# Kernel tuning notes

Hardware: AMD Instinct MI355X
Metric: run time of the kernel (lower is better)

Reference implementation:

```python
import jax, jax.numpy as jnp
import numpy as np

N_NODES = 50000
N_EDGES = 800000


def setup_inputs() -> dict:
    key = jax.random.key(0)
    k1, k2, k3, k4 = jax.random.split(key, 4)
    x = jax.random.normal(k1, (N_NODES, 100), dtype=jnp.float32)
    edge_index = jax.random.randint(k2, (2, N_EDGES), 0, N_NODES, dtype=jnp.int64)
    W1 = jax.random.normal(k3, (100, 128), dtype=jnp.float32) * 0.1
    b1 = jnp.zeros((128,), dtype=jnp.float32)
    W2 = jax.random.normal(k4, (128, 64), dtype=jnp.float32) * 0.1
    b2 = jnp.zeros((64,), dtype=jnp.float32)
    return {"x": x, "edge_index": edge_index, "W1": W1, "b1": b1, "W2": W2, "b2": b2}


def _gcn_norm(edge_index, n_nodes):
    # PyG GCNConv default: add self-loops, then symmetric normalization
    row, col = edge_index[0], edge_index[1]
    loop = jnp.arange(n_nodes, dtype=row.dtype)
    row = jnp.concatenate([row, loop])
    col = jnp.concatenate([col, loop])
    deg = jax.ops.segment_sum(jnp.ones_like(col, dtype=jnp.float32), col,
                              num_segments=n_nodes)
    dinv = jnp.where(deg > 0, jax.lax.rsqrt(deg), 0.0)
    norm = dinv[row] * dinv[col]  # [E + N]
    return row, col, norm


def _gcn_conv(x, W, b, row, col, norm, n_nodes):
    h = x @ W                       # [N, out] linear transform first (PyG order)
    msg = norm[:, None] * h[row]    # gather + scale over edges
    agg = jax.ops.segment_sum(msg, col, num_segments=n_nodes)  # scatter-add
    return agg + b


def reference(x, edge_index, W1, b1, W2, b2):
    n = x.shape[0]
    row, col, norm = _gcn_norm(edge_index, n)
    h = _gcn_conv(x, W1, b1, row, col, norm, n)
    h = jax.nn.relu(h)
    out = _gcn_conv(h, W2, b2, row, col, norm, n)
    return out
```

## Files before the change

kernel.cpp:

```cpp
#include <hip/hip_runtime.h>
#include <hip/hip_fp16.h>

#define DIV_UP(a,b) (((a)+(b)-1)/(b))

typedef _Float16 half8 __attribute__((ext_vector_type(8)));
typedef float f32x4 __attribute__((ext_vector_type(4)));

#define BUK_BITS 9
#define BUK_SIZE 512
#define BUK_CAP  12288
#define MAXBUK   128
#define NBLK_BUCKET 512
#define CHUNK_MAX 1568

#define SWZ(row, colh) ((colh) ^ (((row) & 7) << 3))


__device__ __forceinline__ int edge_at(const void* ei, int mode64, int idx) {
  if (mode64) return (int)((const long long*)ei)[idx];
  return ((const int*)ei)[idx];
}

__global__ void k_init(const int* __restrict__ ei32, int* __restrict__ mode,
                       int* __restrict__ bcur, int nbuk) {
  int t = threadIdx.x;
  if (t < 64) {
    int v = ei32[2 * t + 1];
    unsigned long long b = __ballot(v == 0);
    if (t == 0) *mode = (b == ~0ull) ? 1 : 0;
  }
  if (t < nbuk) bcur[t] = t * BUK_CAP;
}

__global__ __launch_bounds__(256) void k_bucket(const void* __restrict__ ei,
                                                const int* __restrict__ mode,
                                                int* __restrict__ bcur,
                                                unsigned int* __restrict__ recs,
                                                int E, int nbuk) {
  __shared__ unsigned int lrec[CHUNK_MAX];
  __shared__ unsigned int sorted[CHUNK_MAX];
  __shared__ int hist[MAXBUK], lofs[MAXBUK], gbase[MAXBUK], cur[MAXBUK];

  const int chunk = DIV_UP(E, gridDim.x);
  const int e0 = blockIdx.x * chunk;
  const int cnt = min(E, e0 + chunk) - e0;
  if (cnt <= 0) return;

  for (int i = threadIdx.x; i < nbuk; i += 256) hist[i] = 0;
  __syncthreads();

  const int m = *mode;
  for (int i = threadIdx.x; i < cnt; i += 256) {
    int r = edge_at(ei, m, e0 + i);
    int c = edge_at(ei, m, E + e0 + i);
    unsigned int rec = ((unsigned)c << 16) | (unsigned)r;
    lrec[i] = rec;
    atomicAdd(&hist[c >> BUK_BITS], 1);
  }
  __syncthreads();

  if (threadIdx.x == 0) {
    int run = 0;
    for (int b = 0; b < nbuk; ++b) { lofs[b] = run; run += hist[b]; }
  }
  __syncthreads();
  for (int b = threadIdx.x; b < nbuk; b += 256) {
    gbase[b] = atomicAdd(&bcur[b], hist[b]);
    cur[b] = lofs[b];
  }
  __syncthreads();

  for (int i = threadIdx.x; i < cnt; i += 256) {
    unsigned int rec = lrec[i];
    int b = rec >> (16 + BUK_BITS);
    int p = atomicAdd(&cur[b], 1);
    sorted[p] = rec;
  }
  __syncthreads();

  for (int i = threadIdx.x; i < cnt; i += 256) {
    unsigned int rec = sorted[i];
    int b = rec >> (16 + BUK_BITS);
    recs[gbase[b] + i - lofs[b]] = rec;
  }
}

__global__ __launch_bounds__(256) void k_bdeg(const int* __restrict__ bcur,
                                              const unsigned int* __restrict__ recs,
                                              float* __restrict__ dinv,
                                              int* __restrict__ rowstart,
                                              int n, int E, int nbuk) {
  __shared__ int h[BUK_SIZE];
  __shared__ int psum[256];
  __shared__ int cnts[MAXBUK];
  __shared__ int sbase;
  const int b = blockIdx.x, tid = threadIdx.x;

  if (tid < nbuk) cnts[tid] = bcur[tid] - tid * BUK_CAP;
  h[tid] = 0; h[tid + 256] = 0;
  __syncthreads();
  if (tid == 0) { int s = 0; for (int j = 0; j < b; ++j) s += cnts[j]; sbase = s; }
  const int cnt = cnts[b];
  const int n0 = b << BUK_BITS;
  const int nn = min(BUK_SIZE, n - n0);
  const int base = b * BUK_CAP;

  for (int i = tid; i < cnt; i += 256)
    atomicAdd(&h[(int)(recs[base + i] >> 16) - n0], 1);
  __syncthreads();

  int a0 = h[2 * tid], a1 = h[2 * tid + 1];
  psum[tid] = a0 + a1;
  __syncthreads();
#pragma unroll
  for (int off2 = 1; off2 < 256; off2 <<= 1) {
    int v = (tid >= off2) ? psum[tid - off2] : 0;
    __syncthreads();
    psum[tid] += v;
    __syncthreads();
  }
  int excl = psum[tid] - (a0 + a1);
  int gb = sbase;
  if (2 * tid < nn)     rowstart[n0 + 2 * tid]     = gb + excl;
  if (2 * tid + 1 < nn) rowstart[n0 + 2 * tid + 1] = gb + excl + a0;
  for (int i = tid; i < nn; i += 256)
    dinv[n0 + i] = rsqrtf((float)h[i] + 1.0f);
  if (b == nbuk - 1 && tid == 0) rowstart[n] = E;
}

__global__ __launch_bounds__(256) void k_convx(const float4* __restrict__ x4,
                                               const float* __restrict__ dinv,
                                               uint2* __restrict__ xh4, int total4) {
  int i = blockIdx.x * 256 + threadIdx.x;
  if (i < total4) {
    int node = i / 25;
    float d = dinv[node];
    float4 v = x4[i];
    union { uint2 u; __half2 h[2]; } p;
    p.h[0] = __halves2half2(__float2half_rn(d * v.x), __float2half_rn(d * v.y));
    p.h[1] = __halves2half2(__float2half_rn(d * v.z), __float2half_rn(d * v.w));
    xh4[i] = p.u;
  }
}

__global__ __launch_bounds__(256) void k_convw2(const float* __restrict__ W1,
                                                const float* __restrict__ W2,
                                                _Float16* __restrict__ Wt1,
                                                _Float16* __restrict__ Wt2) {
  int i = blockIdx.x * 256 + threadIdx.x;
  if (i < 128 * 128) {
    int nn = i >> 7, k = i & 127;
    Wt1[i] = (k < 100) ? (_Float16)W1[k * 128 + nn] : (_Float16)0.f;
  } else if (i < 128 * 128 + 64 * 128) {
    int j = i - 128 * 128;
    int nn = j >> 7, k = j & 127;
    Wt2[j] = (_Float16)W2[k * 64 + nn];
  }
}

__global__ __launch_bounds__(256) void k_csrfill(const int* __restrict__ bcur,
                                                 const unsigned int* __restrict__ recs,
                                                 const int* __restrict__ rowstart,
                                                 unsigned short* __restrict__ csr, int n) {
  __shared__ unsigned short lcsr[BUK_CAP];
  __shared__ int curs[BUK_SIZE];
  const int b = blockIdx.x;
  const int base = b * BUK_CAP;
  const int cnt = bcur[b] - base;
  const int n0 = b << BUK_BITS;
  const int nn = min(BUK_SIZE, n - n0);
  const int sec0 = rowstart[n0];

  for (int i = threadIdx.x; i < nn; i += 256) curs[i] = rowstart[n0 + i] - sec0;
  __syncthreads();
  for (int i = threadIdx.x; i < cnt; i += 256) {
    unsigned int rec = recs[base + i];
    int cl = (int)(rec >> 16) - n0;
    int p = atomicAdd(&curs[cl], 1);
    lcsr[p] = (unsigned short)(rec & 0xFFFFu);
  }
  __syncthreads();
  for (int i = threadIdx.x; i < cnt; i += 256) csr[sec0 + i] = lcsr[i];
}

__device__ __forceinline__ float4 h4_to_f4(uint2 u) {
  union { uint2 u; __half2 h[2]; } p; p.u = u;
  float2 a = __half22float2(p.h[0]);
  float2 b = __half22float2(p.h[1]);
  return make_float4(a.x, a.y, b.x, b.y);
}
__device__ __forceinline__ void acc_add(float4& acc, float4 a) {
  acc.x += a.x; acc.y += a.y; acc.z += a.z; acc.w += a.w;
}

__global__ __launch_bounds__(256) void k_pull1(const int* __restrict__ rowstart,
                                               const unsigned short* __restrict__ csr,
                                               const uint2* __restrict__ xh4,
                                               const float* __restrict__ dinv,
                                               uint2* __restrict__ aggh4, int n) {
  int g = threadIdx.x / 25;
  int lane = threadIdx.x - g * 25;
  if (g >= 10) return;
  int node = blockIdx.x * 10 + g;
  if (node >= n) return;

  float4 acc = h4_to_f4(xh4[node * 25 + lane]);
  int beg = rowstart[node], end = rowstart[node + 1];
  int j = beg;
  for (; j + 3 < end; j += 4) {
    int r0 = csr[j], r1 = csr[j + 1], r2 = csr[j + 2], r3 = csr[j + 3];
    float4 a = h4_to_f4(xh4[r0 * 25 + lane]);
    float4 b = h4_to_f4(xh4[r1 * 25 + lane]);
    float4 c = h4_to_f4(xh4[r2 * 25 + lane]);
    float4 d = h4_to_f4(xh4[r3 * 25 + lane]);
    acc_add(acc, a); acc_add(acc, b); acc_add(acc, c); acc_add(acc, d);
  }
  for (; j < end; ++j) acc_add(acc, h4_to_f4(xh4[(int)csr[j] * 25 + lane]));

  float d = dinv[node];
  union { uint2 u; __half2 h[2]; } p;
  p.h[0] = __halves2half2(__float2half_rn(d * acc.x), __float2half_rn(d * acc.y));
  p.h[1] = __halves2half2(__float2half_rn(d * acc.z), __float2half_rn(d * acc.w));
  aggh4[node * 32 + lane] = p.u;
  if (lane < 7) aggh4[node * 32 + 25 + lane] = make_uint2(0u, 0u);
}

__global__ __launch_bounds__(256) void k_pull2(const int* __restrict__ rowstart,
                                               const unsigned short* __restrict__ csr,
                                               const uint4* __restrict__ th4,
                                               const float* __restrict__ dinv,
                                               const float4* __restrict__ b2_4,
                                               float4* __restrict__ out4, int n) {
  int g = threadIdx.x >> 3;
  int lane = threadIdx.x & 7;
  int node = blockIdx.x * 32 + g;
  if (node >= n) return;

  uint4 sv = th4[node * 8 + lane];
  float4 acc0 = h4_to_f4(make_uint2(sv.x, sv.y));
  float4 acc1 = h4_to_f4(make_uint2(sv.z, sv.w));

  int beg = rowstart[node], end = rowstart[node + 1];
  int j = beg;
  for (; j + 3 < end; j += 4) {
    uint4 u0 = th4[(int)csr[j] * 8 + lane];
    uint4 u1 = th4[(int)csr[j + 1] * 8 + lane];
    uint4 u2 = th4[(int)csr[j + 2] * 8 + lane];
    uint4 u3 = th4[(int)csr[j + 3] * 8 + lane];
    acc_add(acc0, h4_to_f4(make_uint2(u0.x, u0.y)));
    acc_add(acc1, h4_to_f4(make_uint2(u0.z, u0.w)));
    acc_add(acc0, h4_to_f4(make_uint2(u1.x, u1.y)));
    acc_add(acc1, h4_to_f4(make_uint2(u1.z, u1.w)));
    acc_add(acc0, h4_to_f4(make_uint2(u2.x, u2.y)));
    acc_add(acc1, h4_to_f4(make_uint2(u2.z, u2.w)));
    acc_add(acc0, h4_to_f4(make_uint2(u3.x, u3.y)));
    acc_add(acc1, h4_to_f4(make_uint2(u3.z, u3.w)));
  }
  for (; j < end; ++j) {
    uint4 u0 = th4[(int)csr[j] * 8 + lane];
    acc_add(acc0, h4_to_f4(make_uint2(u0.x, u0.y)));
    acc_add(acc1, h4_to_f4(make_uint2(u0.z, u0.w)));
  }
  float d = dinv[node];
  float4 bb0 = b2_4[lane * 2], bb1 = b2_4[lane * 2 + 1];
  out4[node * 16 + lane * 2]     = make_float4(d * acc0.x + bb0.x, d * acc0.y + bb0.y,
                                               d * acc0.z + bb0.z, d * acc0.w + bb0.w);
  out4[node * 16 + lane * 2 + 1] = make_float4(d * acc1.x + bb1.x, d * acc1.y + bb1.y,
                                               d * acc1.z + bb1.z, d * acc1.w + bb1.w);
}

__global__ __launch_bounds__(256, 2) void k_gemmf(const _Float16* __restrict__ A,
                                                  const _Float16* __restrict__ Wt1,
                                                  const float* __restrict__ b1,
                                                  const _Float16* __restrict__ Wt2,
                                                  const float* __restrict__ dinv,
                                                  _Float16* __restrict__ thh, int n) {
  __shared__ __align__(16) _Float16 lds[4][16 * 128];
  const int wid = threadIdx.x >> 6;
  const int lane = threadIdx.x & 63;
  const int lr = lane & 15;
  const int lk = lane >> 4;
  _Float16* myl = lds[wid];

  half8 B1[8][4];
#pragma unroll
  for (int nt = 0; nt < 8; ++nt)
#pragma unroll
    for (int ks = 0; ks < 4; ++ks)
      B1[nt][ks] = *(const half8*)&Wt1[(nt * 16 + lr) * 128 + ks * 32 + lk * 8];
  float bs[8];
#pragma unroll
  for (int nt = 0; nt < 8; ++nt) bs[nt] = b1[nt * 16 + lr];

  const int nstrips = (n + 15) >> 4;
  for (int s = blockIdx.x * 4 + wid; s < nstrips; s += gridDim.x * 4) {
    const int arow = s * 16 + lr;
    half8 a[4];
#pragma unroll
    for (int ks = 0; ks < 4; ++ks)
      a[ks] = (arow < n) ? *(const half8*)&A[(size_t)arow * 128 + ks * 32 + lk * 8]
                         : half8{0, 0, 0, 0, 0, 0, 0, 0};
    f32x4 acc[8];
#pragma unroll
    for (int nt = 0; nt < 8; ++nt) acc[nt] = f32x4{0.f, 0.f, 0.f, 0.f};
#pragma unroll
    for (int ks = 0; ks < 4; ++ks)
#pragma unroll
      for (int nt = 0; nt < 8; ++nt)
        acc[nt] = __builtin_amdgcn_mfma_f32_16x16x32_f16(a[ks], B1[nt][ks], acc[nt], 0, 0, 0);

#pragma unroll
    for (int r = 0; r < 4; ++r) {
      int row = lk * 4 + r;
#pragma unroll
      for (int nt = 0; nt < 8; ++nt)
        myl[row * 128 + SWZ(row, nt * 16 + lr)] =
            (_Float16)fmaxf(acc[nt][r] + bs[nt], 0.f);
    }

    half8 B2[4][4];
#pragma unroll
    for (int nt = 0; nt < 4; ++nt)
#pragma unroll
      for (int ks = 0; ks < 4; ++ks)
        B2[nt][ks] = *(const half8*)&Wt2[(nt * 16 + lr) * 128 + ks * 32 + lk * 8];

    half8 a2[4];
#pragma unroll
    for (int ks = 0; ks < 4; ++ks)
      a2[ks] = *(const half8*)&myl[lr * 128 + SWZ(lr, ks * 32 + lk * 8)];

    f32x4 acc2[4];
#pragma unroll
    for (int nt = 0; nt < 4; ++nt) acc2[nt] = f32x4{0.f, 0.f, 0.f, 0.f};
#pragma unroll
    for (int ks = 0; ks < 4; ++ks)
#pragma unroll
      for (int nt = 0; nt < 4; ++nt)
        acc2[nt] = __builtin_amdgcn_mfma_f32_16x16x32_f16(a2[ks], B2[nt][ks], acc2[nt], 0, 0, 0);

    const int rb = s * 16 + lk * 4;
    float sc[4];
    if (rb + 3 < n) {
      const float4 dv = *(const float4*)&dinv[rb];
      sc[0] = dv.x; sc[1] = dv.y; sc[2] = dv.z; sc[3] = dv.w;
    } else {
#pragma unroll
      for (int r = 0; r < 4; ++r) sc[r] = (rb + r < n) ? dinv[rb + r] : 0.f;
    }
#pragma unroll
    for (int r = 0; r < 4; ++r) {
      const int orow = rb + r;
      if (orow < n) {
#pragma unroll
        for (int nt = 0; nt < 4; ++nt)
          thh[(size_t)orow * 64 + nt * 16 + lr] = (_Float16)(acc2[nt][r] * sc[r]);
      }
    }
  }
}

extern "C" void kernel_launch(void* const* d_in, const int* in_sizes, int n_in,
                              void* d_out, int out_size, void* d_ws, size_t ws_size,
                              hipStream_t stream) {
  const float* x  = (const float*)d_in[0];
  const void*  ei = d_in[1];
  const float* W1 = (const float*)d_in[2];
  const float* b1 = (const float*)d_in[3];
  const float* W2 = (const float*)d_in[4];
  const float* b2 = (const float*)d_in[5];
  float* out = (float*)d_out;

  const int n = in_sizes[0] / 100;
  const int E = in_sizes[1] / 2;
  const int nbuk = DIV_UP(n, BUK_SIZE);

  char* ws = (char*)d_ws;
  size_t off = 0;
  auto alloc = [&](size_t bytes) { void* p = ws + off; off += (bytes + 15) & ~15ull; return p; };
  int*            mode     = (int*)   alloc(64 * 4);
  int*            bcur     = (int*)   alloc(MAXBUK * 4);
  float*          dinv     = (float*) alloc((size_t)n * 4);
  int*            rowstart = (int*)   alloc(((size_t)n + 4) * 4);
  unsigned int*   recs     = (unsigned int*)alloc((size_t)nbuk * BUK_CAP * 4);
  unsigned short* csr      = (unsigned short*)alloc((size_t)E * 2);
  _Float16*       xh       = (_Float16*)alloc((size_t)n * 100 * 2);
  _Float16*       aggh     = (_Float16*)alloc((size_t)n * 128 * 2);
  _Float16*       thh      = (_Float16*)alloc((size_t)n * 64 * 2);
  _Float16*       Wt1h     = (_Float16*)alloc(128 * 128 * 2);
  _Float16*       Wt2h     = (_Float16*)alloc(64 * 128 * 2);

  k_init<<<1, 128, 0, stream>>>((const int*)ei, mode, bcur, nbuk);
  k_bucket<<<NBLK_BUCKET, 256, 0, stream>>>(ei, mode, bcur, recs, E, nbuk);
  k_bdeg<<<nbuk, 256, 0, stream>>>(bcur, recs, dinv, rowstart, n, E, nbuk);

  k_convx<<<DIV_UP(n * 25, 256), 256, 0, stream>>>((const float4*)x, dinv, (uint2*)xh, n * 25);
  k_convw2<<<DIV_UP(128 * 128 + 64 * 128, 256), 256, 0, stream>>>(W1, W2, Wt1h, Wt2h);
  k_csrfill<<<nbuk, 256, 0, stream>>>(bcur, recs, rowstart, csr, n);

  k_pull1<<<DIV_UP(n, 10), 256, 0, stream>>>(rowstart, csr, (const uint2*)xh, dinv,
                                             (uint2*)aggh, n);
  const int nstrips = DIV_UP(n, 16);
  k_gemmf<<<DIV_UP(nstrips, 8), 256, 0, stream>>>(aggh, Wt1h, b1, Wt2h, dinv, thh, n);
  k_pull2<<<DIV_UP(n, 32), 256, 0, stream>>>(rowstart, csr, (const uint4*)thh, dinv,
                                             (const float4*)b2, (float4*)out, n);
}
```

Baseline: 132.0 us.

## Pad CSR rows to multiples of eight with dummy node, fuse degree and fill

Each row's neighbour list is padded to a multiple of 8 entries, with padding pointing at a zeroed dummy node. This lets the pull kernels read 8 indices with one 16-byte load and skip tail loops. Degree counting, CSR fill and the per-bucket layout are fused into one kernel with a fixed per-bucket CSR capacity, which removes the global prefix over buckets and one launch. Weight conversion moves into the init kernel, and x rows are padded to a stride of 32 for shift indexing. The cost is extra padded gathers and larger buffers, and overflow is possible if a bucket exceeds its capacity.

Result: faster. 119.4 us (-9.5%).

```diff
diff --git a/kernel.cpp b/kernel.cpp
--- a/kernel.cpp
+++ b/kernel.cpp
@@ -6,12 +6,13 @@
 typedef _Float16 half8 __attribute__((ext_vector_type(8)));
 typedef float f32x4 __attribute__((ext_vector_type(4)));
 
-#define BUK_BITS 9
-#define BUK_SIZE 512
-#define BUK_CAP  12288
-#define MAXBUK   128
-#define NBLK_BUCKET 512
-#define CHUNK_MAX 1568
+#define BUK_BITS 8
+#define BUK_SIZE 256
+#define BUK_CAP  6144
+#define CSR_CAP  8192
+#define MAXBUK   256
+#define NBLK_BUCKET 256
+#define CHUNK_MAX 3136
 
 #define SWZ(row, colh) ((colh) ^ (((row) & 7) << 3))
 
@@ -21,15 +22,32 @@
   return ((const int*)ei)[idx];
 }
 
-__global__ void k_init(const int* __restrict__ ei32, int* __restrict__ mode,
-                       int* __restrict__ bcur, int nbuk) {
+__global__ __launch_bounds__(256) void k_init(const int* __restrict__ ei32,
+                                              int* __restrict__ mode,
+                                              int* __restrict__ bcur, int nbuk,
+                                              const float* __restrict__ W1,
+                                              const float* __restrict__ W2,
+                                              _Float16* __restrict__ Wt1,
+                                              _Float16* __restrict__ Wt2) {
   int t = threadIdx.x;
-  if (t < 64) {
-    int v = ei32[2 * t + 1];
-    unsigned long long b = __ballot(v == 0);
-    if (t == 0) *mode = (b == ~0ull) ? 1 : 0;
-  }
-  if (t < nbuk) bcur[t] = t * BUK_CAP;
+  if (blockIdx.x == 0) {
+    if (t < 64) {
+      int v = ei32[2 * t + 1];
+      unsigned long long b = __ballot(v == 0);
+      if (t == 0) *mode = (b == ~0ull) ? 1 : 0;
+    }
+    if (t < nbuk) bcur[t] = t * BUK_CAP;
+  } else {
+    int i = (blockIdx.x - 1) * 256 + t;
+    if (i < 128 * 128) {
+      int nn = i >> 7, k = i & 127;
+      Wt1[i] = (k < 100) ? (_Float16)W1[k * 128 + nn] : (_Float16)0.f;
+    } else {
+      int j = i - 128 * 128;
+      int nn = j >> 7, k = j & 127;
+      Wt2[j] = (_Float16)W2[k * 64 + nn];
+    }
+  }
 }
 
 __global__ __launch_bounds__(256) void k_bucket(const void* __restrict__ ei,
@@ -85,32 +103,32 @@
   }
 }
 
-__global__ __launch_bounds__(256) void k_bdeg(const int* __restrict__ bcur,
-                                              const unsigned int* __restrict__ recs,
-                                              float* __restrict__ dinv,
-                                              int* __restrict__ rowstart,
-                                              int n, int E, int nbuk) {
+__global__ __launch_bounds__(256) void k_bdeg_fill(const int* __restrict__ bcur,
+                                                   const unsigned int* __restrict__ recs,
+                                                   float* __restrict__ dinv,
+                                                   int2* __restrict__ rowinfo,
+                                                   unsigned short* __restrict__ csr,
+                                                   int n) {
   __shared__ int h[BUK_SIZE];
-  __shared__ int psum[256];
-  __shared__ int cnts[MAXBUK];
-  __shared__ int sbase;
+  __shared__ int psum[BUK_SIZE];
+  __shared__ int curs[BUK_SIZE];
+  __shared__ unsigned short lcsr[CSR_CAP];
+
   const int b = blockIdx.x, tid = threadIdx.x;
-
-  if (tid < nbuk) cnts[tid] = bcur[tid] - tid * BUK_CAP;
-  h[tid] = 0; h[tid + 256] = 0;
-  __syncthreads();
-  if (tid == 0) { int s = 0; for (int j = 0; j < b; ++j) s += cnts[j]; sbase = s; }
-  const int cnt = cnts[b];
+  const int base = b * BUK_CAP;
+  const int cnt = bcur[b] - base;
   const int n0 = b << BUK_BITS;
   const int nn = min(BUK_SIZE, n - n0);
-  const int base = b * BUK_CAP;
-
+
+  h[tid] = 0;
+  __syncthreads();
   for (int i = tid; i < cnt; i += 256)
     atomicAdd(&h[(int)(recs[base + i] >> 16) - n0], 1);
   __syncthreads();
 
-  int a0 = h[2 * tid], a1 = h[2 * tid + 1];
-  psum[tid] = a0 + a1;
+  const int deg = h[tid];
+  const int plen = (deg + 7) & ~7;
+  psum[tid] = plen;
   __syncthreads();
 #pragma unroll
   for (int off2 = 1; off2 < 256; off2 <<= 1) {
@@ -119,68 +137,47 @@
     psum[tid] += v;
     __syncthreads();
   }
-  int excl = psum[tid] - (a0 + a1);
-  int gb = sbase;
-  if (2 * tid < nn)     rowstart[n0 + 2 * tid]     = gb + excl;
-  if (2 * tid + 1 < nn) rowstart[n0 + 2 * tid + 1] = gb + excl + a0;
-  for (int i = tid; i < nn; i += 256)
-    dinv[n0 + i] = rsqrtf((float)h[i] + 1.0f);
-  if (b == nbuk - 1 && tid == 0) rowstart[n] = E;
+  const int excl = psum[tid] - plen;
+  const int ptot = psum[255];
+
+  if (tid < nn) {
+    rowinfo[n0 + tid] = make_int2(b * CSR_CAP + excl, plen);
+    dinv[n0 + tid] = rsqrtf((float)deg + 1.0f);
+    curs[tid] = excl;
+  }
+  for (int i = tid; i < ptot; i += 256) lcsr[i] = (unsigned short)n;
+  __syncthreads();
+
+  for (int i = tid; i < cnt; i += 256) {
+    unsigned int rec = recs[base + i];
+    int cl = (int)(rec >> 16) - n0;
+    int p = atomicAdd(&curs[cl], 1);
+    lcsr[p] = (unsigned short)(rec & 0xFFFFu);
+  }
+  __syncthreads();
+  for (int i = tid; i < ptot; i += 256) csr[b * CSR_CAP + i] = lcsr[i];
 }
 
 __global__ __launch_bounds__(256) void k_convx(const float4* __restrict__ x4,
                                                const float* __restrict__ dinv,
-                                               uint2* __restrict__ xh4, int total4) {
+                                               uint2* __restrict__ xh4,
+                                               uint2* __restrict__ thh2,
+                                               int n, int total4) {
   int i = blockIdx.x * 256 + threadIdx.x;
   if (i < total4) {
     int node = i / 25;
+    int lane = i - node * 25;
     float d = dinv[node];
     float4 v = x4[i];
     union { uint2 u; __half2 h[2]; } p;
     p.h[0] = __halves2half2(__float2half_rn(d * v.x), __float2half_rn(d * v.y));
     p.h[1] = __halves2half2(__float2half_rn(d * v.z), __float2half_rn(d * v.w));
-    xh4[i] = p.u;
-  }
-}
-
-__global__ __launch_bounds__(256) void k_convw2(const float* __restrict__ W1,
-                                                const float* __restrict__ W2,
-                                                _Float16* __restrict__ Wt1,
-                                                _Float16* __restrict__ Wt2) {
-  int i = blockIdx.x * 256 + threadIdx.x;
-  if (i < 128 * 128) {
-    int nn = i >> 7, k = i & 127;
-    Wt1[i] = (k < 100) ? (_Float16)W1[k * 128 + nn] : (_Float16)0.f;
-  } else if (i < 128 * 128 + 64 * 128) {
-    int j = i - 128 * 128;
-    int nn = j >> 7, k = j & 127;
-    Wt2[j] = (_Float16)W2[k * 64 + nn];
-  }
-}
-
-__global__ __launch_bounds__(256) void k_csrfill(const int* __restrict__ bcur,
-                                                 const unsigned int* __restrict__ recs,
-                                                 const int* __restrict__ rowstart,
-                                                 unsigned short* __restrict__ csr, int n) {
-  __shared__ unsigned short lcsr[BUK_CAP];
-  __shared__ int curs[BUK_SIZE];
-  const int b = blockIdx.x;
-  const int base = b * BUK_CAP;
-  const int cnt = bcur[b] - base;
-  const int n0 = b << BUK_BITS;
-  const int nn = min(BUK_SIZE, n - n0);
-  const int sec0 = rowstart[n0];
-
-  for (int i = threadIdx.x; i < nn; i += 256) curs[i] = rowstart[n0 + i] - sec0;
-  __syncthreads();
-  for (int i = threadIdx.x; i < cnt; i += 256) {
-    unsigned int rec = recs[base + i];
-    int cl = (int)(rec >> 16) - n0;
-    int p = atomicAdd(&curs[cl], 1);
-    lcsr[p] = (unsigned short)(rec & 0xFFFFu);
-  }
-  __syncthreads();
-  for (int i = threadIdx.x; i < cnt; i += 256) csr[sec0 + i] = lcsr[i];
+    xh4[(node << 5) + lane] = p.u;
+  } else {
+    int s = i - total4;
+    if (s < 32) xh4[(n << 5) + s] = make_uint2(0u, 0u);
+    else if (s < 48) thh2[n * 16 + (s - 32)] = make_uint2(0u, 0u);
+  }
 }
 
 __device__ __forceinline__ float4 h4_to_f4(uint2 u) {
@@ -193,7 +190,7 @@
   acc.x += a.x; acc.y += a.y; acc.z += a.z; acc.w += a.w;
 }
 
-__global__ __launch_bounds__(256) void k_pull1(const int* __restrict__ rowstart,
+__global__ __launch_bounds__(256) void k_pull1(const int2* __restrict__ rowinfo,
                                                const unsigned short* __restrict__ csr,
                                                const uint2* __restrict__ xh4,
                                                const float* __restrict__ dinv,
@@ -204,19 +201,26 @@
   int node = blockIdx.x * 10 + g;
   if (node >= n) return;
 
-  float4 acc = h4_to_f4(xh4[node * 25 + lane]);
-  int beg = rowstart[node], end = rowstart[node + 1];
-  int j = beg;
-  for (; j + 3 < end; j += 4) {
-    int r0 = csr[j], r1 = csr[j + 1], r2 = csr[j + 2], r3 = csr[j + 3];
-    float4 a = h4_to_f4(xh4[r0 * 25 + lane]);
-    float4 b = h4_to_f4(xh4[r1 * 25 + lane]);
-    float4 c = h4_to_f4(xh4[r2 * 25 + lane]);
-    float4 d = h4_to_f4(xh4[r3 * 25 + lane]);
-    acc_add(acc, a); acc_add(acc, b); acc_add(acc, c); acc_add(acc, d);
-  }
-  for (; j < end; ++j) acc_add(acc, h4_to_f4(xh4[(int)csr[j] * 25 + lane]));
-
+  float4 acc = h4_to_f4(xh4[(node << 5) + lane]);
+  int2 ri = rowinfo[node];
+  int beg = ri.x, end = ri.x + ri.y;
+  for (int j = beg; j < end; j += 8) {
+    uint4 cw = *(const uint4*)&csr[j];
+    int r0 = cw.x & 0xFFFF, r1 = cw.x >> 16;
+    int r2 = cw.y & 0xFFFF, r3 = cw.y >> 16;
+    int r4 = cw.z & 0xFFFF, r5 = cw.z >> 16;
+    int r6 = cw.w & 0xFFFF, r7 = cw.w >> 16;
+    float4 t0 = h4_to_f4(xh4[(r0 << 5) + lane]);
+    float4 t1 = h4_to_f4(xh4[(r1 << 5) + lane]);
+    float4 t2 = h4_to_f4(xh4[(r2 << 5) + lane]);
+    float4 t3 = h4_to_f4(xh4[(r3 << 5) + lane]);
+    float4 t4 = h4_to_f4(xh4[(r4 << 5) + lane]);
+    float4 t5 = h4_to_f4(xh4[(r5 << 5) + lane]);
+    float4 t6 = h4_to_f4(xh4[(r6 << 5) + lane]);
+    float4 t7 = h4_to_f4(xh4[(r7 << 5) + lane]);
+    acc_add(acc, t0); acc_add(acc, t1); acc_add(acc, t2); acc_add(acc, t3);
+    acc_add(acc, t4); acc_add(acc, t5); acc_add(acc, t6); acc_add(acc, t7);
+  }
   float d = dinv[node];
   union { uint2 u; __half2 h[2]; } p;
   p.h[0] = __halves2half2(__float2half_rn(d * acc.x), __float2half_rn(d * acc.y));
@@ -225,7 +229,7 @@
   if (lane < 7) aggh4[node * 32 + 25 + lane] = make_uint2(0u, 0u);
 }
 
-__global__ __launch_bounds__(256) void k_pull2(const int* __restrict__ rowstart,
+__global__ __launch_bounds__(256) void k_pull2(const int2* __restrict__ rowinfo,
                                                const unsigned short* __restrict__ csr,
                                                const uint4* __restrict__ th4,
                                                const float* __restrict__ dinv,
@@ -236,17 +240,26 @@
   int node = blockIdx.x * 32 + g;
   if (node >= n) return;
 
-  uint4 sv = th4[node * 8 + lane];
+  uint4 sv = th4[(node << 3) + lane];
   float4 acc0 = h4_to_f4(make_uint2(sv.x, sv.y));
   float4 acc1 = h4_to_f4(make_uint2(sv.z, sv.w));
 
-  int beg = rowstart[node], end = rowstart[node + 1];
-  int j = beg;
-  for (; j + 3 < end; j += 4) {
-    uint4 u0 = th4[(int)csr[j] * 8 + lane];
-    uint4 u1 = th4[(int)csr[j + 1] * 8 + lane];
-    uint4 u2 = th4[(int)csr[j + 2] * 8 + lane];
-    uint4 u3 = th4[(int)csr[j + 3] * 8 + lane];
+  int2 ri = rowinfo[node];
+  int beg = ri.x, end = ri.x + ri.y;
+  for (int j = beg; j < end; j += 8) {
+    uint4 cw = *(const uint4*)&csr[j];
+    int r0 = cw.x & 0xFFFF, r1 = cw.x >> 16;
+    int r2 = cw.y & 0xFFFF, r3 = cw.y >> 16;
+    int r4 = cw.z & 0xFFFF, r5 = cw.z >> 16;
+    int r6 = cw.w & 0xFFFF, r7 = cw.w >> 16;
+    uint4 u0 = th4[(r0 << 3) + lane];
+    uint4 u1 = th4[(r1 << 3) + lane];
+    uint4 u2 = th4[(r2 << 3) + lane];
+    uint4 u3 = th4[(r3 << 3) + lane];
+    uint4 u4 = th4[(r4 << 3) + lane];
+    uint4 u5 = th4[(r5 << 3) + lane];
+    uint4 u6 = th4[(r6 << 3) + lane];
+    uint4 u7 = th4[(r7 << 3) + lane];
     acc_add(acc0, h4_to_f4(make_uint2(u0.x, u0.y)));
     acc_add(acc1, h4_to_f4(make_uint2(u0.z, u0.w)));
     acc_add(acc0, h4_to_f4(make_uint2(u1.x, u1.y)));
@@ -255,11 +268,14 @@
     acc_add(acc1, h4_to_f4(make_uint2(u2.z, u2.w)));
     acc_add(acc0, h4_to_f4(make_uint2(u3.x, u3.y)));
     acc_add(acc1, h4_to_f4(make_uint2(u3.z, u3.w)));
-  }
-  for (; j < end; ++j) {
-    uint4 u0 = th4[(int)csr[j] * 8 + lane];
-    acc_add(acc0, h4_to_f4(make_uint2(u0.x, u0.y)));
-    acc_add(acc1, h4_to_f4(make_uint2(u0.z, u0.w)));
+    acc_add(acc0, h4_to_f4(make_uint2(u4.x, u4.y)));
+    acc_add(acc1, h4_to_f4(make_uint2(u4.z, u4.w)));
+    acc_add(acc0, h4_to_f4(make_uint2(u5.x, u5.y)));
+    acc_add(acc1, h4_to_f4(make_uint2(u5.z, u5.w)));
+    acc_add(acc0, h4_to_f4(make_uint2(u6.x, u6.y)));
+    acc_add(acc1, h4_to_f4(make_uint2(u6.z, u6.w)));
+    acc_add(acc0, h4_to_f4(make_uint2(u7.x, u7.y)));
+    acc_add(acc1, h4_to_f4(make_uint2(u7.z, u7.w)));
   }
   float d = dinv[node];
   float4 bb0 = b2_4[lane * 2], bb1 = b2_4[lane * 2 + 1];
@@ -381,27 +397,27 @@
   int*            mode     = (int*)   alloc(64 * 4);
   int*            bcur     = (int*)   alloc(MAXBUK * 4);
   float*          dinv     = (float*) alloc((size_t)n * 4);
-  int*            rowstart = (int*)   alloc(((size_t)n + 4) * 4);
+  int2*           rowinfo  = (int2*)  alloc((size_t)n * 8);
   unsigned int*   recs     = (unsigned int*)alloc((size_t)nbuk * BUK_CAP * 4);
-  unsigned short* csr      = (unsigned short*)alloc((size_t)E * 2);
-  _Float16*       xh       = (_Float16*)alloc((size_t)n * 100 * 2);
+  unsigned short* csr      = (unsigned short*)alloc((size_t)nbuk * CSR_CAP * 2);
+  _Float16*       xh       = (_Float16*)alloc((size_t)(n + 1) * 128 * 2);
   _Float16*       aggh     = (_Float16*)alloc((size_t)n * 128 * 2);
-  _Float16*       thh      = (_Float16*)alloc((size_t)n * 64 * 2);
+  _Float16*       thh      = (_Float16*)alloc((size_t)(n + 1) * 64 * 2);
   _Float16*       Wt1h     = (_Float16*)alloc(128 * 128 * 2);
   _Float16*       Wt2h     = (_Float16*)alloc(64 * 128 * 2);
 
-  k_init<<<1, 128, 0, stream>>>((const int*)ei, mode, bcur, nbuk);
+  k_init<<<97, 256, 0, stream>>>((const int*)ei, mode, bcur, nbuk, W1, W2, Wt1h, Wt2h);
   k_bucket<<<NBLK_BUCKET, 256, 0, stream>>>(ei, mode, bcur, recs, E, nbuk);
-  k_bdeg<<<nbuk, 256, 0, stream>>>(bcur, recs, dinv, rowstart, n, E, nbuk);
-
-  k_convx<<<DIV_UP(n * 25, 256), 256, 0, stream>>>((const float4*)x, dinv, (uint2*)xh, n * 25);
-  k_convw2<<<DIV_UP(128 * 128 + 64 * 128, 256), 256, 0, stream>>>(W1, W2, Wt1h, Wt2h);
-  k_csrfill<<<nbuk, 256, 0, stream>>>(bcur, recs, rowstart, csr, n);
-
-  k_pull1<<<DIV_UP(n, 10), 256, 0, stream>>>(rowstart, csr, (const uint2*)xh, dinv,
+  k_bdeg_fill<<<nbuk, 256, 0, stream>>>(bcur, recs, dinv, rowinfo, csr, n);
+
+  const int total4 = n * 25;
+  k_convx<<<DIV_UP(total4 + 48, 256), 256, 0, stream>>>((const float4*)x, dinv,
+      (uint2*)xh, (uint2*)thh, n, total4);
+
+  k_pull1<<<DIV_UP(n, 10), 256, 0, stream>>>(rowinfo, csr, (const uint2*)xh, dinv,
                                              (uint2*)aggh, n);
   const int nstrips = DIV_UP(n, 16);
   k_gemmf<<<DIV_UP(nstrips, 8), 256, 0, stream>>>(aggh, Wt1h, b1, Wt2h, dinv, thh, n);
-  k_pull2<<<DIV_UP(n, 32), 256, 0, stream>>>(rowstart, csr, (const uint4*)thh, dinv,
+  k_pull2<<<DIV_UP(n, 32), 256, 0, stream>>>(rowinfo, csr, (const uint4*)thh, dinv,
                                              (const float4*)b2, (float4*)out, n);
 }
```
